# Performance work log

Hardware: AMD Instinct MI355X
Metric: run time of the kernel (lower is better)

## Reference

```python
import jax, jax.numpy as jnp
import numpy as np

BASE = 7.0  # ModularPhaseNorm base

def apply_rot(x, ang):
    """Apply num_rotation_planes learnable 2D rotations to the leading 2*P dims of x (eidosTransform input rotation)."""
    P = ang.shape[-1]
    c = jnp.cos(ang); s = jnp.sin(ang)
    x0 = x[..., 0:2 * P:2]; x1 = x[..., 1:2 * P:2]
    head = jnp.stack([c * x0 - s * x1, s * x0 + c * x1], axis=-1).reshape(x.shape[:-1] + (2 * P,))
    return jnp.concatenate([head, x[..., 2 * P:]], axis=-1)

def pnorm(x, g, b):
    """ModularPhaseNorm: wrap activations mod `base`, rescale to [-1,1], learnable affine."""
    return g * ((jnp.mod(x, BASE) - BASE / 2) / (BASE / 2)) + b

def setup_inputs() -> dict:
    key = jax.random.key(0)
    ks = jax.random.split(key, 12)
    B, F, T, S = 4096, 512, 9, 9
    H1, H2 = 32, 64
    return {
        'path_data': jax.random.normal(ks[0], (B, F, T * S), jnp.float32),
        'W1': jax.random.normal(ks[1], (T, H1, F), jnp.float32) * (1.0 / np.sqrt(F)),
        'b1': jnp.zeros((T, H1), jnp.float32),
        'ang1': jax.random.normal(ks[2], (T, 2), jnp.float32) * 0.1,
        'gamma1': jnp.ones((T, H1), jnp.float32),
        'beta1': jnp.zeros((T, H1), jnp.float32),
        'W2': jax.random.normal(ks[3], (T, H1), jnp.float32) * (1.0 / np.sqrt(H1)),
        'b2': jnp.zeros((T,), jnp.float32),
        'ang2': jax.random.normal(ks[4], (T, 2), jnp.float32) * 0.1,
        'mW1': jax.random.normal(ks[5], (H2, F), jnp.float32) * (1.0 / np.sqrt(F)),
        'mb1': jnp.zeros((H2,), jnp.float32),
        'mang1': jax.random.normal(ks[6], (4,), jnp.float32) * 0.1,
        'mgamma': jnp.ones((H2,), jnp.float32),
        'mbeta': jnp.zeros((H2,), jnp.float32),
        'mW2': jax.random.normal(ks[7], (H2,), jnp.float32) * (1.0 / np.sqrt(H2)),
        'mb2': jnp.zeros((), jnp.float32),
        'mang2': jax.random.normal(ks[8], (2,), jnp.float32) * 0.1,
        'comm_coeff': jnp.asarray(0.05, jnp.float32),
        'res_coeff': jnp.asarray(0.02, jnp.float32),
        'int_coeff': jnp.asarray(0.03, jnp.float32),
    }

def reference(path_data, W1, b1, ang1, gamma1, beta1, W2, b2, ang2,
              mW1, mb1, mang1, mgamma, mbeta, mW2, mb2, mang2,
              comm_coeff, res_coeff, int_coeff):
    B, F, NP = path_data.shape
    T = W1.shape[0]; S = NP // T
    # contiguous team slices -> [B, T, S, F]; all num_teams*team_size tiny scorers fused into batched einsums
    x = path_data.reshape(B, F, T, S).transpose(0, 2, 3, 1)
    # per-team PathTeamScorer: eidosTransform(F->32, 2 planes) -> ModularPhaseNorm(32) -> eidosTransform(32->1, 2 planes)
    h = apply_rot(x, ang1[None, :, None, :])
    h = jnp.einsum('btsf,tof->btso', h, W1) + b1[None, :, None, :]
    h = pnorm(h, gamma1[None, :, None, :], beta1[None, :, None, :])
    h = apply_rot(h, ang2[None, :, None, :])
    scores = jnp.einsum('btso,to->bts', h, W2) + b2[None, :, None]
    q = jax.nn.softmax(scores, axis=-1)                      # within-team quality [B,T,S]
    team_out = jnp.einsum('btsf,bts->btf', x, q)             # softmax-weighted pooling
    # meta scorer over team outputs: F->64 (4 planes) -> phase-norm -> 64->1 (2 planes)
    hm = apply_rot(team_out, mang1)
    hm = jnp.einsum('btf,of->bto', hm, mW1) + mb1
    hm = pnorm(hm, mgamma, mbeta)
    hm = apply_rot(hm, mang2)
    ms = jnp.einsum('bto,o->bt', hm, mW2) + mb2
    mw = jax.nn.softmax(ms, axis=1)                          # [B,T]
    final = jnp.einsum('btf,bt->bf', team_out, mw)
    # CoordinationOverhead
    tq = q.mean(axis=-1)                                     # [B,T] team mean qualities
    mean = tq.mean(axis=1, keepdims=True)
    var = jnp.var(tq, axis=1, ddof=1, keepdims=True)         # torch unbiased var
    nv = var / (mean ** 2 + 1e-8)
    total = comm_coeff * T * (T - 1) / 2 + res_coeff * T + (int_coeff * T * (1.0 + nv)).reshape(-1)
    pen = jnp.minimum(total, 0.5)
    return final * (1.0 - pen)[:, None]
```

## Files before the change

kernel.cpp:

```cpp
#include <hip/hip_runtime.h>
#include <cmath>

constexpr int kF   = 512;
constexpr int kT   = 9;
constexpr int kS   = 9;
constexpr int kNP  = 81;
constexpr int kH1  = 32;
constexpr int kH2  = 64;
constexpr int kBLK = 576;

constexpr int WS_W1P  = 0;
constexpr int WS_W2P  = WS_W1P + kT * kF * kH1;
constexpr int WS_MW1P = WS_W2P + kT * kH1;
constexpr int WS_MW2P = WS_MW1P + kF * kH2;
constexpr int WS_TOTAL = WS_MW2P + kH2;

constexpr int kFCH = 64;
constexpr int kNCH = kF / kFCH;

constexpr int SM_XBUF = 0;
constexpr int SM_TO   = SM_XBUF + kFCH*kNP;
constexpr int SM_Q    = SM_TO + kT*kF;
constexpr int SM_TQ   = SM_Q + kT*12;
constexpr int SM_MS   = SM_TQ + 12;
constexpr int SM_MW   = SM_MS + 12;
constexpr int SM_SCALE= SM_MW + 12;
constexpr int SM_FLOATS = SM_SCALE + 4;

typedef float vf4 __attribute__((ext_vector_type(4)));

__device__ __forceinline__ float pnorm1(float x, float g, float b) {
    float r = fmodf(x, 7.0f);
    if (r < 0.0f) r += 7.0f;
    return g * ((r - 3.5f) / 3.5f) + b;
}

__global__ void prep_kernel(const float* __restrict__ W1, const float* __restrict__ ang1,
                            const float* __restrict__ W2, const float* __restrict__ ang2,
                            const float* __restrict__ mW1, const float* __restrict__ mang1,
                            const float* __restrict__ mW2, const float* __restrict__ mang2,
                            float* __restrict__ ws) {
    int i = blockIdx.x * 256 + threadIdx.x;
    if (i < kT * kF * kH1) {
        int t = i / (kF * kH1); int r = i - t * (kF * kH1);
        int f = r / kH1;        int o = r - f * kH1;
        float v;
        if (f >= 4) {
            v = W1[(t * kH1 + o) * kF + f];
        } else {
            int p = f >> 1; float a = ang1[t * 2 + p];
            float c = cosf(a), s = sinf(a);
            float w0 = W1[(t * kH1 + o) * kF + 2 * p];
            float w1 = W1[(t * kH1 + o) * kF + 2 * p + 1];
            v = (f & 1) ? (-s * w0 + c * w1) : (c * w0 + s * w1);
        }
        ws[WS_W1P + (t * kF + f) * kH1 + o] = v;
    }
    int j = i - kT * kF * kH1;
    if (j >= 0 && j < kT * kH1) {
        int t = j / kH1, o = j - (j / kH1) * kH1;
        float v;
        if (o >= 4) {
            v = W2[t * kH1 + o];
        } else {
            int p = o >> 1; float a = ang2[t * 2 + p];
            float c = cosf(a), s = sinf(a);
            float w0 = W2[t * kH1 + 2 * p], w1 = W2[t * kH1 + 2 * p + 1];
            v = (o & 1) ? (-s * w0 + c * w1) : (c * w0 + s * w1);
        }
        ws[WS_W2P + j] = v;
    }
    int k = j - kT * kH1;
    if (k >= 0 && k < kF * kH2) {
        int f = k / kH2, o = k - (k / kH2) * kH2;
        float v;
        if (f >= 8) {
            v = mW1[o * kF + f];
        } else {
            int p = f >> 1; float a = mang1[p];
            float c = cosf(a), s = sinf(a);
            float w0 = mW1[o * kF + 2 * p], w1 = mW1[o * kF + 2 * p + 1];
            v = (f & 1) ? (-s * w0 + c * w1) : (c * w0 + s * w1);
        }
        ws[WS_MW1P + f * kH2 + o] = v;
    }
    int m = k - kF * kH2;
    if (m >= 0 && m < kH2) {
        float v;
        if (m >= 4) {
            v = mW2[m];
        } else {
            int p = m >> 1; float a = mang2[p];
            float c = cosf(a), s = sinf(a);
            float w0 = mW2[2 * p], w1 = mW2[2 * p + 1];
            v = (m & 1) ? (-s * w0 + c * w1) : (c * w0 + s * w1);
        }
        ws[WS_MW2P + m] = v;
    }
}

__global__ __launch_bounds__(kBLK) void scorer_kernel(
    const float* __restrict__ path,  const float* __restrict__ b1,
    const float* __restrict__ gamma1, const float* __restrict__ beta1,
    const float* __restrict__ b2v,   const float* __restrict__ mb1,
    const float* __restrict__ mgamma, const float* __restrict__ mbeta,
    const float* __restrict__ mb2,   const float* __restrict__ c_comm,
    const float* __restrict__ c_res, const float* __restrict__ c_int,
    const float* __restrict__ ws,    float* __restrict__ out) {
    __shared__ float sm[SM_FLOATS];
    const int tid = threadIdx.x;
    const int b   = blockIdx.x;
    const int wv  = tid >> 6;
    const int ln  = tid & 63;
    const int o   = ln & 31;
    const int fh  = ln >> 5;
    const float* W1p  = ws + WS_W1P;
    const float* W2p  = ws + WS_W2P;
    const float* mW1p = ws + WS_MW1P;
    const float* mW2p = ws + WS_MW2P;
    const size_t pbase = (size_t)b * (kF * kNP);

    float acc[kS];
    #pragma unroll
    for (int s = 0; s < kS; ++s) acc[s] = 0.f;
    {
        const float* xp = path + pbase + (size_t)(fh * (kF / 2)) * kNP + wv * kS;
        const float* wp = W1p + ((size_t)wv * kF + fh * (kF / 2)) * kH1 + o;
        #pragma unroll 2
        for (int f = 0; f < kF / 2; ++f) {
            float w = wp[f * kH1];
            const float* xr = xp + f * kNP;
            #pragma unroll
            for (int s = 0; s < kS; ++s) acc[s] += xr[s] * w;
        }
    }
    #pragma unroll
    for (int s = 0; s < kS; ++s) acc[s] += __shfl_xor(acc[s], 32);

    {
        const float bb = b1[wv * kH1 + o];
        const float gg = gamma1[wv * kH1 + o];
        const float be = beta1[wv * kH1 + o];
        const float w2 = W2p[wv * kH1 + o];
        float con[kS];
        #pragma unroll
        for (int s = 0; s < kS; ++s) con[s] = pnorm1(acc[s] + bb, gg, be) * w2;
        #pragma unroll
        for (int s = 0; s < kS; ++s) {
            con[s] += __shfl_xor(con[s], 1);
            con[s] += __shfl_xor(con[s], 2);
            con[s] += __shfl_xor(con[s], 4);
            con[s] += __shfl_xor(con[s], 8);
            con[s] += __shfl_xor(con[s], 16);
        }
        const float b2t = b2v[wv];
        float sc[kS];
        #pragma unroll
        for (int s = 0; s < kS; ++s) sc[s] = con[s] + b2t;
        float mx = sc[0];
        #pragma unroll
        for (int s = 1; s < kS; ++s) mx = fmaxf(mx, sc[s]);
        float e[kS]; float sum = 0.f;
        #pragma unroll
        for (int s = 0; s < kS; ++s) { e[s] = expf(sc[s] - mx); sum += e[s]; }
        const float inv = 1.f / sum;
        if (ln == 0) {
            float tqv = 0.f;
            #pragma unroll
            for (int s = 0; s < kS; ++s) {
                float qv = e[s] * inv;
                sm[SM_Q + wv * 12 + s] = qv;
                tqv += qv;
            }
            sm[SM_TQ + wv] = tqv * (1.f / 9.f);
        }
    }
    __syncthreads();

    float qr[kS];
    #pragma unroll
    for (int s = 0; s < kS; ++s) qr[s] = sm[SM_Q + wv * 12 + s];

    for (int ch = 0; ch < kNCH; ++ch) {
        if (ch) __syncthreads();
        const float* g = path + pbase + (size_t)ch * (kFCH * kNP);
        for (int i = tid; i < (kFCH * kNP) / 4; i += kBLK) {
            ((vf4*)(sm + SM_XBUF))[i] = ((const vf4*)g)[i];
        }
        __syncthreads();
        const float* xp = sm + SM_XBUF + ln * kNP + wv * kS;
        float v = 0.f;
        #pragma unroll
        for (int s = 0; s < kS; ++s) v += xp[s] * qr[s];
        sm[SM_TO + wv * kF + ch * kFCH + ln] = v;
    }
    __syncthreads();

    {
        const int f0 = wv * 57;
        const int f1 = (wv == 8) ? kF : f0 + 57;
        float am[kT];
        #pragma unroll
        for (int t = 0; t < kT; ++t) am[t] = 0.f;
        for (int f = f0; f < f1; ++f) {
            float w = mW1p[f * kH2 + ln];
            #pragma unroll
            for (int t = 0; t < kT; ++t) am[t] += sm[SM_TO + t * kF + f] * w;
        }
        #pragma unroll
        for (int t = 0; t < kT; ++t) sm[SM_XBUF + (wv * kT + t) * 64 + ln] = am[t];
    }
    __syncthreads();
    {
        float h = mb1[ln];
        #pragma unroll
        for (int w = 0; w < kT; ++w) h += sm[SM_XBUF + (w * kT + wv) * 64 + ln];
        float val = pnorm1(h, mgamma[ln], mbeta[ln]) * mW2p[ln];
        val += __shfl_xor(val, 1);
        val += __shfl_xor(val, 2);
        val += __shfl_xor(val, 4);
        val += __shfl_xor(val, 8);
        val += __shfl_xor(val, 16);
        val += __shfl_xor(val, 32);
        if (ln == 0) sm[SM_MS + wv] = val + mb2[0];
    }
    __syncthreads();
    if (tid == 0) {
        float mx = -1e30f;
        for (int t = 0; t < kT; ++t) mx = fmaxf(mx, sm[SM_MS + t]);
        float e[kT]; float sum = 0.f;
        for (int t = 0; t < kT; ++t) { e[t] = expf(sm[SM_MS + t] - mx); sum += e[t]; }
        float inv = 1.f / sum;
        for (int t = 0; t < kT; ++t) sm[SM_MW + t] = e[t] * inv;
        float mean = 0.f;
        for (int t = 0; t < kT; ++t) mean += sm[SM_TQ + t];
        mean *= (1.f / 9.f);
        float var = 0.f;
        for (int t = 0; t < kT; ++t) { float d = sm[SM_TQ + t] - mean; var += d * d; }
        var *= (1.f / 8.f);
        float nv = var / (mean * mean + 1e-8f);
        float total = c_comm[0] * (kT * (kT - 1) / 2) + c_res[0] * kT +
                      c_int[0] * kT * (1.f + nv);
        float pen = fminf(total, 0.5f);
        sm[SM_SCALE] = 1.f - pen;
    }
    __syncthreads();

    {
        float mwr[kT];
        #pragma unroll
        for (int t = 0; t < kT; ++t) mwr[t] = sm[SM_MW + t];
        const float scl = sm[SM_SCALE];
        if (tid < kF) {
            float v = 0.f;
            #pragma unroll
            for (int t = 0; t < kT; ++t) v += sm[SM_TO + t * kF + tid] * mwr[t];
            out[(size_t)b * kF + tid] = v * scl;
        }
    }
}

extern "C" void kernel_launch(void* const* d_in, const int* in_sizes, int n_in,
                              void* d_out, int out_size, void* d_ws, size_t ws_size,
                              hipStream_t stream) {
    const float* path   = (const float*)d_in[0];
    const float* W1     = (const float*)d_in[1];
    const float* b1     = (const float*)d_in[2];
    const float* ang1   = (const float*)d_in[3];
    const float* gamma1 = (const float*)d_in[4];
    const float* beta1  = (const float*)d_in[5];
    const float* W2     = (const float*)d_in[6];
    const float* b2     = (const float*)d_in[7];
    const float* ang2   = (const float*)d_in[8];
    const float* mW1    = (const float*)d_in[9];
    const float* mb1    = (const float*)d_in[10];
    const float* mang1  = (const float*)d_in[11];
    const float* mgamma = (const float*)d_in[12];
    const float* mbeta  = (const float*)d_in[13];
    const float* mW2    = (const float*)d_in[14];
    const float* mb2    = (const float*)d_in[15];
    const float* mang2  = (const float*)d_in[16];
    const float* c_comm = (const float*)d_in[17];
    const float* c_res  = (const float*)d_in[18];
    const float* c_int  = (const float*)d_in[19];
    float* ws = (float*)d_ws;
    float* outp = (float*)d_out;

    const int Bn = in_sizes[0] / (kF * kNP);

    prep_kernel<<<(WS_TOTAL + 255) / 256, 256, 0, stream>>>(
        W1, ang1, W2, ang2, mW1, mang1, mW2, mang2, ws);
    scorer_kernel<<<Bn, kBLK, 0, stream>>>(
        path, b1, gamma1, beta1, b2, mb1, mgamma, mbeta, mb2,
        c_comm, c_res, c_int, ws, outp);
}
```

Measured before the change: 1.905 ms.

## Stage path tiles into LDS with async double-buffered loads and register-block W1

The first team-scorer GEMM no longer reads the path tile straight from global memory with strided scalar loads. It now pulls 32-feature chunks into two LDS buffers using global_load_lds, prefetching the next chunk while the current one is consumed. Each lane now accumulates four hidden outputs as a vf4, so cross-lane reductions shrink and the softmax qualities stay in registers instead of going through LDS. The pooling pass reuses the same double-buffered staging, with two half-waves splitting the slot dimension. In exchange it depends on LDS-DMA addressing and wait semantics being handled correctly, and it adds more barriers and register pressure.

```diff
diff --git a/kernel.cpp b/kernel.cpp
--- a/kernel.cpp
+++ b/kernel.cpp
@@ -15,16 +15,18 @@
 constexpr int WS_MW2P = WS_MW1P + kF * kH2;
 constexpr int WS_TOTAL = WS_MW2P + kH2;
 
-constexpr int kFCH = 64;
-constexpr int kNCH = kF / kFCH;
-
-constexpr int SM_XBUF = 0;
-constexpr int SM_TO   = SM_XBUF + kFCH*kNP;
-constexpr int SM_Q    = SM_TO + kT*kF;
-constexpr int SM_TQ   = SM_Q + kT*12;
-constexpr int SM_MS   = SM_TQ + 12;
-constexpr int SM_MW   = SM_MS + 12;
-constexpr int SM_SCALE= SM_MW + 12;
+constexpr int kCHF  = 32;
+constexpr int kNCH  = kF / kCHF;
+constexpr int kCHFL = kCHF * kNP;
+constexpr int kCHV4 = kCHFL / 4;
+
+constexpr int SM_XB0 = 0;
+constexpr int SM_XB1 = kCHFL;
+constexpr int SM_TO  = 2 * kCHFL;
+constexpr int SM_TQ  = SM_TO + kT * kF;
+constexpr int SM_MS  = SM_TQ + 12;
+constexpr int SM_MW  = SM_MS + 12;
+constexpr int SM_SCALE = SM_MW + 12;
 constexpr int SM_FLOATS = SM_SCALE + 4;
 
 typedef float vf4 __attribute__((ext_vector_type(4)));
@@ -33,6 +35,16 @@
     float r = fmodf(x, 7.0f);
     if (r < 0.0f) r += 7.0f;
     return g * ((r - 3.5f) / 3.5f) + b;
+}
+
+__device__ __forceinline__ void stage_chunk(const float* __restrict__ g,
+                                            float* lds_base, int tid) {
+    for (int i = tid; i < kCHV4; i += kBLK) {
+        __builtin_amdgcn_global_load_lds(
+            (const __attribute__((address_space(1))) void*)(g + i * 4),
+            (__attribute__((address_space(3))) void*)(lds_base + i * 4),
+            16, 0, 0);
+    }
 }
 
 __global__ void prep_kernel(const float* __restrict__ W1, const float* __restrict__ ang1,
@@ -112,87 +124,107 @@
     const int b   = blockIdx.x;
     const int wv  = tid >> 6;
     const int ln  = tid & 63;
-    const int o   = ln & 31;
-    const int fh  = ln >> 5;
     const float* W1p  = ws + WS_W1P;
     const float* W2p  = ws + WS_W2P;
     const float* mW1p = ws + WS_MW1P;
     const float* mW2p = ws + WS_MW2P;
     const size_t pbase = (size_t)b * (kF * kNP);
-
-    float acc[kS];
+    const float* xrow = path + pbase;
+
+    const int og = ln & 7;
+    const int fl = ln >> 3;
+    vf4 acc[kS];
     #pragma unroll
-    for (int s = 0; s < kS; ++s) acc[s] = 0.f;
-    {
-        const float* xp = path + pbase + (size_t)(fh * (kF / 2)) * kNP + wv * kS;
-        const float* wp = W1p + ((size_t)wv * kF + fh * (kF / 2)) * kH1 + o;
-        #pragma unroll 2
-        for (int f = 0; f < kF / 2; ++f) {
-            float w = wp[f * kH1];
-            const float* xr = xp + f * kNP;
+    for (int s = 0; s < kS; ++s) acc[s] = (vf4){0.f, 0.f, 0.f, 0.f};
+
+    stage_chunk(xrow, sm + SM_XB0, tid);
+    for (int ch = 0; ch < kNCH; ++ch) {
+        __syncthreads();
+        if (ch + 1 < kNCH)
+            stage_chunk(xrow + (ch + 1) * kCHFL,
+                        sm + (((ch + 1) & 1) ? SM_XB1 : SM_XB0), tid);
+        const float* bufp  = sm + ((ch & 1) ? SM_XB1 : SM_XB0);
+        const float* wbase = W1p + ((size_t)(wv * kF + ch * kCHF)) * kH1 + og * 4;
+        #pragma unroll
+        for (int k = 0; k < kCHF / 8; ++k) {
+            const int flc = k * 8 + fl;
+            const vf4 w = *(const vf4*)(wbase + flc * kH1);
+            const float* xr = bufp + flc * kNP + wv * kS;
             #pragma unroll
-            for (int s = 0; s < kS; ++s) acc[s] += xr[s] * w;
-        }
-    }
+            for (int s = 0; s < kS; ++s) {
+                const float xv = xr[s];
+                acc[s].x += xv * w.x; acc[s].y += xv * w.y;
+                acc[s].z += xv * w.z; acc[s].w += xv * w.w;
+            }
+        }
+    }
+
     #pragma unroll
-    for (int s = 0; s < kS; ++s) acc[s] += __shfl_xor(acc[s], 32);
-
-    {
-        const float bb = b1[wv * kH1 + o];
-        const float gg = gamma1[wv * kH1 + o];
-        const float be = beta1[wv * kH1 + o];
-        const float w2 = W2p[wv * kH1 + o];
+    for (int s = 0; s < kS; ++s) {
+        #pragma unroll
+        for (int m = 8; m <= 32; m <<= 1) {
+            acc[s].x += __shfl_xor(acc[s].x, m);
+            acc[s].y += __shfl_xor(acc[s].y, m);
+            acc[s].z += __shfl_xor(acc[s].z, m);
+            acc[s].w += __shfl_xor(acc[s].w, m);
+        }
+    }
+
+    float qr[kS];
+    {
+        const int ob = wv * kH1 + og * 4;
+        const vf4 bb = *(const vf4*)(b1 + ob);
+        const vf4 gg = *(const vf4*)(gamma1 + ob);
+        const vf4 be = *(const vf4*)(beta1 + ob);
+        const vf4 w2 = *(const vf4*)(W2p + ob);
         float con[kS];
         #pragma unroll
-        for (int s = 0; s < kS; ++s) con[s] = pnorm1(acc[s] + bb, gg, be) * w2;
+        for (int s = 0; s < kS; ++s) {
+            con[s] = pnorm1(acc[s].x + bb.x, gg.x, be.x) * w2.x +
+                     pnorm1(acc[s].y + bb.y, gg.y, be.y) * w2.y +
+                     pnorm1(acc[s].z + bb.z, gg.z, be.z) * w2.z +
+                     pnorm1(acc[s].w + bb.w, gg.w, be.w) * w2.w;
+        }
         #pragma unroll
         for (int s = 0; s < kS; ++s) {
             con[s] += __shfl_xor(con[s], 1);
             con[s] += __shfl_xor(con[s], 2);
             con[s] += __shfl_xor(con[s], 4);
-            con[s] += __shfl_xor(con[s], 8);
-            con[s] += __shfl_xor(con[s], 16);
         }
         const float b2t = b2v[wv];
-        float sc[kS];
-        #pragma unroll
-        for (int s = 0; s < kS; ++s) sc[s] = con[s] + b2t;
-        float mx = sc[0];
-        #pragma unroll
-        for (int s = 1; s < kS; ++s) mx = fmaxf(mx, sc[s]);
-        float e[kS]; float sum = 0.f;
-        #pragma unroll
-        for (int s = 0; s < kS; ++s) { e[s] = expf(sc[s] - mx); sum += e[s]; }
+        float mx = con[0] + b2t;
+        #pragma unroll
+        for (int s = 1; s < kS; ++s) mx = fmaxf(mx, con[s] + b2t);
+        float sum = 0.f;
+        #pragma unroll
+        for (int s = 0; s < kS; ++s) { qr[s] = expf(con[s] + b2t - mx); sum += qr[s]; }
         const float inv = 1.f / sum;
-        if (ln == 0) {
-            float tqv = 0.f;
-            #pragma unroll
-            for (int s = 0; s < kS; ++s) {
-                float qv = e[s] * inv;
-                sm[SM_Q + wv * 12 + s] = qv;
-                tqv += qv;
-            }
-            sm[SM_TQ + wv] = tqv * (1.f / 9.f);
-        }
-    }
-    __syncthreads();
-
-    float qr[kS];
-    #pragma unroll
-    for (int s = 0; s < kS; ++s) qr[s] = sm[SM_Q + wv * 12 + s];
-
+        float tqv = 0.f;
+        #pragma unroll
+        for (int s = 0; s < kS; ++s) { qr[s] *= inv; tqv += qr[s]; }
+        if (ln == 0) sm[SM_TQ + wv] = tqv * (1.f / 9.f);
+    }
+
+    const int fP = ln & 31, sh = ln >> 5;
+    float qh[5];
+    {
+        const int sbase = sh * 4;
+        #pragma unroll
+        for (int jq = 0; jq < 5; ++jq) qh[jq] = qr[sbase + jq];
+        if (sh == 1) qh[0] = 0.f;
+    }
+    stage_chunk(xrow, sm + SM_XB0, tid);
     for (int ch = 0; ch < kNCH; ++ch) {
-        if (ch) __syncthreads();
-        const float* g = path + pbase + (size_t)ch * (kFCH * kNP);
-        for (int i = tid; i < (kFCH * kNP) / 4; i += kBLK) {
-            ((vf4*)(sm + SM_XBUF))[i] = ((const vf4*)g)[i];
-        }
         __syncthreads();
-        const float* xp = sm + SM_XBUF + ln * kNP + wv * kS;
-        float v = 0.f;
-        #pragma unroll
-        for (int s = 0; s < kS; ++s) v += xp[s] * qr[s];
-        sm[SM_TO + wv * kF + ch * kFCH + ln] = v;
+        if (ch + 1 < kNCH)
+            stage_chunk(xrow + (ch + 1) * kCHFL,
+                        sm + (((ch + 1) & 1) ? SM_XB1 : SM_XB0), tid);
+        const float* bufp = sm + ((ch & 1) ? SM_XB1 : SM_XB0);
+        const float* xr = bufp + fP * kNP + wv * kS + sh * 4;
+        float v = xr[0] * qh[0] + xr[1] * qh[1] + xr[2] * qh[2] +
+                  xr[3] * qh[3] + xr[4] * qh[4];
+        v += __shfl_xor(v, 32);
+        if (sh == 0) sm[SM_TO + wv * kF + ch * kCHF + fP] = v;
     }
     __syncthreads();
 
@@ -208,13 +240,13 @@
             for (int t = 0; t < kT; ++t) am[t] += sm[SM_TO + t * kF + f] * w;
         }
         #pragma unroll
-        for (int t = 0; t < kT; ++t) sm[SM_XBUF + (wv * kT + t) * 64 + ln] = am[t];
+        for (int t = 0; t < kT; ++t) sm[SM_XB0 + (wv * kT + t) * 64 + ln] = am[t];
     }
     __syncthreads();
     {
         float h = mb1[ln];
         #pragma unroll
-        for (int w = 0; w < kT; ++w) h += sm[SM_XBUF + (w * kT + wv) * 64 + ln];
+        for (int w = 0; w < kT; ++w) h += sm[SM_XB0 + (w * kT + wv) * 64 + ln];
         float val = pnorm1(h, mgamma[ln], mbeta[ln]) * mW2p[ln];
         val += __shfl_xor(val, 1);
         val += __shfl_xor(val, 2);
```

After: 1.595 ms. 16.2% less time.
